# Optimization experiments

Hardware: AMD Instinct MI355X
Metric: run time of the kernel (lower is better)

Reference implementation:

```python
import jax, jax.numpy as jnp
import numpy as np

N_EMBD = 1024
N_HEAD = 16
HEAD_DIM = N_EMBD // N_HEAD


def setup_inputs() -> dict:
    key = jax.random.key(0)
    ks = jax.random.split(key, 9)
    B, T, C = 2, 2048, N_EMBD
    s = 1.0 / np.sqrt(C)
    inp = {
        "x": jax.random.normal(ks[0], (B, T, C), dtype=jnp.float32),
        "Wq": jax.random.normal(ks[1], (C, C), dtype=jnp.float32) * s,
        "bq": jnp.zeros((C,), dtype=jnp.float32),
        "Wk": jax.random.normal(ks[2], (C, C), dtype=jnp.float32) * s,
        "bk": jnp.zeros((C,), dtype=jnp.float32),
        "Wv": jax.random.normal(ks[3], (C, C), dtype=jnp.float32) * s,
        "bv": jnp.zeros((C,), dtype=jnp.float32),
        "Wo": jax.random.normal(ks[4], (C, C), dtype=jnp.float32) * s,
        "bo": jnp.zeros((C,), dtype=jnp.float32),
    }
    return inp


def reference(x, Wq, bq, Wk, bk, Wv, bv, Wo, bo):
    B, T, C = x.shape
    H, D = N_HEAD, HEAD_DIM
    # projections (torch Linear: x @ W^T + b)
    q = (x @ Wq.T + bq).reshape(B, T, H, D).transpose(0, 2, 1, 3)  # [B,H,T,D]
    k = (x @ Wk.T + bk).reshape(B, T, H, D).transpose(0, 2, 1, 3)
    v = (x @ Wv.T + bv).reshape(B, T, H, D).transpose(0, 2, 1, 3)
    scores = jnp.einsum("bhqd,bhkd->bhqk", q, k) / jnp.sqrt(jnp.asarray(D, x.dtype))
    causal = jnp.tril(jnp.ones((T, T), dtype=bool))
    scores = jnp.where(causal[None, None], scores, jnp.asarray(-jnp.inf, x.dtype))
    weights = jax.nn.softmax(scores, axis=-1)  # [B,H,T,T]
    attended = jnp.einsum("bhqk,bhkd->bhqd", weights, v)
    attended = attended.transpose(0, 2, 1, 3).reshape(B, T, C)
    return attended @ Wo.T + bo
```

## Files before the change

kernel.cpp:

```cpp
#include <hip/hip_runtime.h>

typedef unsigned short u16;
typedef __attribute__((ext_vector_type(8))) __bf16 bf16x8;
typedef __attribute__((ext_vector_type(4))) float f32x4;
typedef __attribute__((ext_vector_type(4))) unsigned int u32x4;

#define MFMA16(a, b, c) __builtin_amdgcn_mfma_f32_16x16x32_bf16(a, b, c, 0, 0, 0)

__device__ __forceinline__ u16 f2bf(float f) {
    unsigned u = __float_as_uint(f);
    u = (u + 0x7FFFu + ((u >> 16) & 1u)) >> 16;
    return (u16)u;
}

__device__ __forceinline__ void gl_lds16(const u16* g, u16* l) {
    __builtin_amdgcn_global_load_lds(
        (const __attribute__((address_space(1))) unsigned int*)g,
        (__attribute__((address_space(3))) unsigned int*)l, 16, 0, 0);
}

static constexpr int Bv = 2, Tv = 2048, Cv = 1024, Hv = 16, Dv = 64;
static constexpr int Mv = Bv * Tv;

static constexpr size_t OFF_XB = 0;
static constexpr size_t OFF_WQ = 4194304;
static constexpr size_t OFF_WK = OFF_WQ + 1048576;
static constexpr size_t OFF_WV = OFF_WK + 1048576;
static constexpr size_t OFF_WO = OFF_WV + 1048576;
static constexpr size_t OFF_Q  = OFF_WO + 1048576;
static constexpr size_t OFF_K  = OFF_Q + 4194304;
static constexpr size_t OFF_VT = OFF_K + 4194304;
static constexpr size_t OFF_A  = OFF_VT + 4194304;

__global__ __launch_bounds__(256) void convert_all(
    const float* __restrict__ x,
    const float* __restrict__ wq, const float* __restrict__ wk,
    const float* __restrict__ wv, const float* __restrict__ wo,
    u16* __restrict__ dst)
{
    int i4 = blockIdx.x * blockDim.x + threadIdx.x;
    if (i4 >= 2097152) return;
    int idx = i4 * 4;
    const float* src; int off;
    if (idx < 4194304) { src = x; off = idx; }
    else {
        int rel = idx - 4194304;
        int j = rel >> 20;
        off = rel & 1048575;
        src = (j == 0) ? wq : (j == 1) ? wk : (j == 2) ? wv : wo;
    }
    float4 v = *(const float4*)(src + off);
    ushort4 o;
    o.x = f2bf(v.x); o.y = f2bf(v.y); o.z = f2bf(v.z); o.w = f2bf(v.w);
    *(ushort4*)(dst + idx) = o;
}

template <bool OUT_BF16, bool ROWBIAS>
__device__ __forceinline__ void gemm128_b64(
    u16* __restrict__ lA0, u16* __restrict__ lB0,
    u16* __restrict__ lA1, u16* __restrict__ lB1,
    const u16* __restrict__ A, const u16* __restrict__ Wt,
    const float* __restrict__ bias, void* __restrict__ outp,
    int m0, int n0, int N, int K)
{
    const int tid  = threadIdx.x;
    const int lane = tid & 63, w = tid >> 6;
    const int quad = lane >> 4, lm = lane & 15;
    const int wm = (w & 1) * 64, wn = (w >> 1) * 32;
    const int rowi = lane >> 3, seg = lane & 7;

    f32x4 zero = {0.f, 0.f, 0.f, 0.f};
    f32x4 acc[4][2];
    #pragma unroll
    for (int mt = 0; mt < 4; mt++)
        #pragma unroll
        for (int nt = 0; nt < 2; nt++) acc[mt][nt] = zero;

    auto stage = [&](u16* dA, u16* dB, int k0) __attribute__((always_inline)) {
        #pragma unroll
        for (int i = 0; i < 2; i++) {
            int rbase = w * 16 + i * 8;
            int row = rbase + rowi;
            int gseg = seg ^ (row & 7);
            gl_lds16(A  + (size_t)(m0 + row) * K + k0 + gseg * 8, &dA[rbase * 64]);
            gl_lds16(Wt + (size_t)(n0 + row) * K + k0 + gseg * 8, &dB[rbase * 64]);
        }
    };
    auto compute = [&](const u16* sA, const u16* sB) __attribute__((always_inline)) {
        #pragma unroll
        for (int ks = 0; ks < 2; ks++) {
            const int swz = ((ks * 4 + quad) ^ (lm & 7)) * 8;
            bf16x8 af[4], bf[2];
            #pragma unroll
            for (int mt = 0; mt < 4; mt++)
                af[mt] = *(const bf16x8*)&sA[(wm + mt * 16 + lm) * 64 + swz];
            #pragma unroll
            for (int nt = 0; nt < 2; nt++)
                bf[nt] = *(const bf16x8*)&sB[(wn + nt * 16 + lm) * 64 + swz];
            #pragma unroll
            for (int mt = 0; mt < 4; mt++)
                #pragma unroll
                for (int nt = 0; nt < 2; nt++)
                    acc[mt][nt] = MFMA16(af[mt], bf[nt], acc[mt][nt]);
        }
    };

    const int NT = K >> 6;
    stage(lA0, lB0, 0);
    stage(lA1, lB1, 64);
    for (int t = 0; t < NT; ++t) {
        if (t + 1 < NT) asm volatile("s_waitcnt vmcnt(4)" ::: "memory");
        else            asm volatile("s_waitcnt vmcnt(0)" ::: "memory");
        __builtin_amdgcn_s_barrier();
        u16* sA = (t & 1) ? lA1 : lA0;
        u16* sB = (t & 1) ? lB1 : lB0;
        compute(sA, sB);
        asm volatile("s_waitcnt lgkmcnt(0)" ::: "memory");
        __builtin_amdgcn_s_barrier();
        if (t + 2 < NT) stage(sA, sB, (t + 2) << 6);
    }

    #pragma unroll
    for (int nt = 0; nt < 2; nt++) {
        int col = n0 + wn + nt * 16 + lm;
        float cb = ROWBIAS ? 0.f : bias[col];
        #pragma unroll
        for (int mt = 0; mt < 4; mt++) {
            #pragma unroll
            for (int r = 0; r < 4; r++) {
                int row = m0 + wm + mt * 16 + quad * 4 + r;
                float v = acc[mt][nt][r] + (ROWBIAS ? bias[row] : cb);
                if (OUT_BF16) ((u16*)outp)[(size_t)row * N + col] = f2bf(v);
                else          ((float*)outp)[(size_t)row * N + col] = v;
            }
        }
    }
}

__global__ __launch_bounds__(512) void gemm_qkv(
    const u16* __restrict__ A,
    const u16* __restrict__ Wq, const u16* __restrict__ Wk, const u16* __restrict__ Wv,
    const float* __restrict__ bq, const float* __restrict__ bk, const float* __restrict__ bv,
    u16* __restrict__ Q, u16* __restrict__ K, u16* __restrict__ VT)
{
    __shared__ u16 lA0[128 * 64];
    __shared__ u16 lB0[128 * 64];
    __shared__ u16 lA1[128 * 64];
    __shared__ u16 lB1[128 * 64];

    int bid = blockIdx.x;
    int sw  = (bid & 7) * 96 + (bid >> 3);
    int g2  = sw >> 5;
    int row = sw & 31;
    int which = g2 >> 3, col = g2 & 7;

    if (which == 0) {
        gemm128_b64<true, false>(lA0, lB0, lA1, lB1, A, Wq, bq, Q, row * 128, col * 128, Cv, Cv);
    } else if (which == 1) {
        gemm128_b64<true, false>(lA0, lB0, lA1, lB1, A, Wk, bk, K, row * 128, col * 128, Cv, Cv);
    } else {
        gemm128_b64<true, true>(lA0, lB0, lA1, lB1, Wv, A, bv, VT, col * 128, row * 128, Mv, Cv);
    }
}

__global__ __launch_bounds__(512) void gemm_o64(
    const u16* __restrict__ A, const u16* __restrict__ Wt,
    const float* __restrict__ bias, float* __restrict__ outp)
{
    __shared__ u16 lA0[128 * 64];
    __shared__ u16 lA1[128 * 64];
    __shared__ u16 lB0[64 * 64];
    __shared__ u16 lB1[64 * 64];

    const int tid  = threadIdx.x;
    const int lane = tid & 63, w = tid >> 6;
    const int quad = lane >> 4, lm = lane & 15;
    const int wm = (w & 3) * 32, wn = (w >> 2) * 32;

    int bid = blockIdx.x;
    int sw  = (bid & 7) * 64 + (bid >> 3);
    const int n0 = (sw >> 5) * 64;
    const int m0 = (sw & 31) * 128;
    const int K = Cv;
    const int rowi = lane >> 3, seg = lane & 7;

    f32x4 zero = {0.f, 0.f, 0.f, 0.f};
    f32x4 acc[2][2];
    #pragma unroll
    for (int mt = 0; mt < 2; mt++)
        #pragma unroll
        for (int nt = 0; nt < 2; nt++) acc[mt][nt] = zero;

    auto stage = [&](u16* dA, u16* dB, int k0) __attribute__((always_inline)) {
        #pragma unroll
        for (int i = 0; i < 2; i++) {
            int rbase = w * 16 + i * 8;
            int row = rbase + rowi;
            int gseg = seg ^ (row & 7);
            gl_lds16(A + (size_t)(m0 + row) * K + k0 + gseg * 8, &dA[rbase * 64]);
        }
        {
            int rbase = w * 8, row = rbase + rowi;
            gl_lds16(Wt + (size_t)(n0 + row) * K + k0 + ((seg ^ (row & 7))) * 8, &dB[rbase * 64]);
        }
    };
    auto compute = [&](const u16* sA, const u16* sB) __attribute__((always_inline)) {
        #pragma unroll
        for (int ks = 0; ks < 2; ks++) {
            const int swz = ((ks * 4 + quad) ^ (lm & 7)) * 8;
            bf16x8 af[2], bf[2];
            #pragma unroll
            for (int mt = 0; mt < 2; mt++)
                af[mt] = *(const bf16x8*)&sA[(wm + mt * 16 + lm) * 64 + swz];
            #pragma unroll
            for (int nt = 0; nt < 2; nt++)
                bf[nt] = *(const bf16x8*)&sB[(wn + nt * 16 + lm) * 64 + swz];
            #pragma unroll
            for (int mt = 0; mt < 2; mt++)
                #pragma unroll
                for (int nt = 0; nt < 2; nt++)
                    acc[mt][nt] = MFMA16(af[mt], bf[nt], acc[mt][nt]);
        }
    };

    const int NT = K >> 6;
    stage(lA0, lB0, 0);
    stage(lA1, lB1, 64);
    for (int t = 0; t < NT; ++t) {
        if (t + 1 < NT) asm volatile("s_waitcnt vmcnt(3)" ::: "memory");
        else            asm volatile("s_waitcnt vmcnt(0)" ::: "memory");
        __builtin_amdgcn_s_barrier();
        u16* sA = (t & 1) ? lA1 : lA0;
        u16* sB = (t & 1) ? lB1 : lB0;
        compute(sA, sB);
        asm volatile("s_waitcnt lgkmcnt(0)" ::: "memory");
        __builtin_amdgcn_s_barrier();
        if (t + 2 < NT) stage(sA, sB, (t + 2) << 6);
    }

    #pragma unroll
    for (int nt = 0; nt < 2; nt++) {
        int col = n0 + wn + nt * 16 + lm;
        float bvv = bias[col];
        #pragma unroll
        for (int mt = 0; mt < 2; mt++) {
            #pragma unroll
            for (int r = 0; r < 4; r++) {
                int row = m0 + wm + mt * 16 + quad * 4 + r;
                outp[(size_t)row * Cv + col] = acc[mt][nt][r] + bvv;
            }
        }
    }
}

__global__ __launch_bounds__(512) void attn(
    const u16* __restrict__ Qp, const u16* __restrict__ Kp,
    const u16* __restrict__ VTg, u16* __restrict__ Op)
{
    __shared__ u16 lK[2][64 * 64];
    __shared__ u16 lVT[2][64 * 64];
    __shared__ u16 lP[8][32][72];

    const int tid  = threadIdx.x;
    const int lane = tid & 63, w = tid >> 6;
    const int g = w >> 2, wl = w & 3;
    const int quad = lane >> 4, lm = lane & 15;

    const int idx  = blockIdx.x;
    const int half = idx >> 8;
    const int grp  = idx & 255;
    const int bh   = (half << 4) | (grp >> 4);
    const int j    = grp & 15;
    const int qt   = half ? j : 15 - j;
    const int h = bh & 15, b = bh >> 4;

    const int qb = qt * 128;
    const size_t headoff = (size_t)b * Tv * Cv + (size_t)h * Dv;
    const size_t vthead  = (size_t)h * 64 * Mv + (size_t)b * Tv;

    bf16x8 qf[2][2];
    #pragma unroll
    for (int nt = 0; nt < 2; nt++) {
        const u16* qptr = Qp + headoff + (size_t)(qb + wl * 32 + nt * 16 + lm) * Cv + quad * 8;
        qf[0][nt] = *(const bf16x8*)(qptr);
        qf[1][nt] = *(const bf16x8*)(qptr + 32);
    }

    f32x4 zero = {0.f, 0.f, 0.f, 0.f};
    f32x4 oacc[2][4];
    #pragma unroll
    for (int mt = 0; mt < 2; mt++)
        #pragma unroll
        for (int nt = 0; nt < 4; nt++) oacc[mt][nt] = zero;
    float Lp[2] = {0.f, 0.f};

    const float SC = 0.18033688011112042f;
    const int rowi = lane >> 3, seg = lane & 7;

    auto stage = [&](int kt) {
        const int k0 = kt * 64;
        #pragma unroll
        for (int hf = 0; hf < 2; hf++) {
            int rbase = wl * 16 + hf * 8;
            int row = rbase + rowi;
            int gseg = seg ^ (row & 7);
            gl_lds16(Kp + headoff + (size_t)(k0 + row) * Cv + gseg * 8, &lK[g][rbase * 64]);
            gl_lds16(VTg + vthead + (size_t)row * Mv + k0 + gseg * 8, &lVT[g][rbase * 64]);
        }
    };

    auto body = [&](int kt, bool domask) __attribute__((always_inline)) {
        const int k0 = kt * 64;
        f32x4 stt[4][2];
        #pragma unroll
        for (int mt = 0; mt < 4; mt++)
            #pragma unroll
            for (int nt = 0; nt < 2; nt++) stt[mt][nt] = zero;
        #pragma unroll
        for (int ks = 0; ks < 2; ks++) {
            #pragma unroll
            for (int mt = 0; mt < 4; mt++) {
                bf16x8 kf = *(const bf16x8*)
                    &lK[g][(mt * 16 + lm) * 64 + (((ks * 4 + quad) ^ (lm & 7)) * 8)];
                #pragma unroll
                for (int nt = 0; nt < 2; nt++)
                    stt[mt][nt] = MFMA16(kf, qf[ks][nt], stt[mt][nt]);
            }
        }
        #pragma unroll
        for (int mt = 0; mt < 4; mt++) {
            #pragma unroll
            for (int nt = 0; nt < 2; nt++) {
                const int keyb = k0 + mt * 16 + quad * 4;
                const int qrow = qb + wl * 32 + nt * 16 + lm;
                float e0 = __builtin_amdgcn_exp2f(fmaf(stt[mt][nt][0], SC, -16.f));
                float e1 = __builtin_amdgcn_exp2f(fmaf(stt[mt][nt][1], SC, -16.f));
                float e2 = __builtin_amdgcn_exp2f(fmaf(stt[mt][nt][2], SC, -16.f));
                float e3 = __builtin_amdgcn_exp2f(fmaf(stt[mt][nt][3], SC, -16.f));
                if (domask) {
                    if (keyb + 0 > qrow) e0 = 0.f;
                    if (keyb + 1 > qrow) e1 = 0.f;
                    if (keyb + 2 > qrow) e2 = 0.f;
                    if (keyb + 3 > qrow) e3 = 0.f;
                }
                Lp[nt] += e0 + e1 + e2 + e3;
                ushort4 pk;
                pk.x = (u16)(__float_as_uint(e0) >> 16);
                pk.y = (u16)(__float_as_uint(e1) >> 16);
                pk.z = (u16)(__float_as_uint(e2) >> 16);
                pk.w = (u16)(__float_as_uint(e3) >> 16);
                *(ushort4*)&lP[w][nt * 16 + lm][mt * 16 + quad * 4] = pk;
            }
        }
        #pragma unroll
        for (int ks = 0; ks < 2; ks++) {
            bf16x8 pf[2];
            #pragma unroll
            for (int mt = 0; mt < 2; mt++)
                pf[mt] = *(const bf16x8*)&lP[w][mt * 16 + lm][ks * 32 + quad * 8];
            #pragma unroll
            for (int nt = 0; nt < 4; nt++) {
                bf16x8 vf = *(const bf16x8*)
                    &lVT[g][(nt * 16 + lm) * 64 + (((ks * 4 + quad) ^ (lm & 7)) * 8)];
                #pragma unroll
                for (int mt = 0; mt < 2; mt++)
                    oacc[mt][nt] = MFMA16(pf[mt], vf, oacc[mt][nt]);
            }
        }
    };

    for (int i = 0; i < qt; i++) {
        if (i) __syncthreads();
        stage(2 * i + g);
        __syncthreads();
        body(2 * i + g, false);
    }
    if (qt) __syncthreads();
    stage(2 * qt + g);
    __syncthreads();
    body(2 * qt + g, true);
    __syncthreads();

    float* lO = (float*)&lP[0][0][0];
    float* lL = lO + 32 * 256;
    const int t = tid & 255;
    if (g == 1) {
        #pragma unroll
        for (int mt = 0; mt < 2; mt++)
            #pragma unroll
            for (int nt = 0; nt < 4; nt++)
                #pragma unroll
                for (int r = 0; r < 4; r++)
                    lO[(mt * 16 + nt * 4 + r) * 256 + t] = oacc[mt][nt][r];
        lL[t] = Lp[0];
        lL[256 + t] = Lp[1];
    }
    __syncthreads();
    if (g == 0) {
        #pragma unroll
        for (int mt = 0; mt < 2; mt++)
            #pragma unroll
            for (int nt = 0; nt < 4; nt++)
                #pragma unroll
                for (int r = 0; r < 4; r++)
                    oacc[mt][nt][r] += lO[(mt * 16 + nt * 4 + r) * 256 + t];
        Lp[0] += lL[t];
        Lp[1] += lL[256 + t];

        float Lred[2];
        #pragma unroll
        for (int nt = 0; nt < 2; nt++) {
            float L = Lp[nt];
            L += __shfl_xor(L, 16, 64);
            L += __shfl_xor(L, 32, 64);
            Lred[nt] = 1.0f / L;
        }
        #pragma unroll
        for (int mt = 0; mt < 2; mt++) {
            float inv[4];
            #pragma unroll
            for (int r = 0; r < 4; r++)
                inv[r] = __shfl(Lred[mt], (lane & 48) | (quad * 4 + r), 64);
            #pragma unroll
            for (int nt = 0; nt < 4; nt++) {
                #pragma unroll
                for (int r = 0; r < 4; r++) {
                    int row = qb + wl * 32 + mt * 16 + quad * 4 + r;
                    Op[headoff + (size_t)row * Cv + nt * 16 + lm] = f2bf(oacc[mt][nt][r] * inv[r]);
                }
            }
        }
    }
}

extern "C" void kernel_launch(void* const* d_in, const int* in_sizes, int n_in,
                              void* d_out, int out_size, void* d_ws, size_t ws_size,
                              hipStream_t stream) {
    const float* x  = (const float*)d_in[0];
    const float* Wq = (const float*)d_in[1];
    const float* bq = (const float*)d_in[2];
    const float* Wk = (const float*)d_in[3];
    const float* bk = (const float*)d_in[4];
    const float* Wv = (const float*)d_in[5];
    const float* bv = (const float*)d_in[6];
    const float* Wo = (const float*)d_in[7];
    const float* bo = (const float*)d_in[8];
    u16* ws = (u16*)d_ws;

    convert_all<<<8192, 256, 0, stream>>>(x, Wq, Wk, Wv, Wo, ws);

    gemm_qkv<<<768, 512, 0, stream>>>(
        ws + OFF_XB, ws + OFF_WQ, ws + OFF_WK, ws + OFF_WV,
        bq, bk, bv, ws + OFF_Q, ws + OFF_K, ws + OFF_VT);

    attn<<<512, 512, 0, stream>>>(ws + OFF_Q, ws + OFF_K, ws + OFF_VT, ws + OFF_A);

    gemm_o64<<<512, 512, 0, stream>>>(ws + OFF_A, ws + OFF_WO, bo, (float*)d_out);
}
```

Before: 173.3 us.

## Restructure QKV GEMM to 256-thread blocks with K=32 steps and packed LDS

```diff
diff --git a/kernel.cpp b/kernel.cpp
--- a/kernel.cpp
+++ b/kernel.cpp
@@ -56,7 +56,7 @@
 }
 
 template <bool OUT_BF16, bool ROWBIAS>
-__device__ __forceinline__ void gemm128_b64(
+__device__ __forceinline__ void gemm128_b32(
     u16* __restrict__ lA0, u16* __restrict__ lB0,
     u16* __restrict__ lA1, u16* __restrict__ lB1,
     const u16* __restrict__ A, const u16* __restrict__ Wt,
@@ -66,62 +66,60 @@
     const int tid  = threadIdx.x;
     const int lane = tid & 63, w = tid >> 6;
     const int quad = lane >> 4, lm = lane & 15;
-    const int wm = (w & 1) * 64, wn = (w >> 1) * 32;
+    const int wm = (w & 1) * 64, wn = (w >> 1) * 64;
+    const int h4A = (w & 1) * 4, h4B = ((w >> 1) & 1) * 4;
     const int rowi = lane >> 3, seg = lane & 7;
+    const int raw = seg ^ rowi;
+    const int hh  = raw >> 2, qq = raw & 3;
 
     f32x4 zero = {0.f, 0.f, 0.f, 0.f};
-    f32x4 acc[4][2];
+    f32x4 acc[4][4];
     #pragma unroll
     for (int mt = 0; mt < 4; mt++)
         #pragma unroll
-        for (int nt = 0; nt < 2; nt++) acc[mt][nt] = zero;
+        for (int nt = 0; nt < 4; nt++) acc[mt][nt] = zero;
 
     auto stage = [&](u16* dA, u16* dB, int k0) __attribute__((always_inline)) {
         #pragma unroll
-        for (int i = 0; i < 2; i++) {
-            int rbase = w * 16 + i * 8;
-            int row = rbase + rowi;
-            int gseg = seg ^ (row & 7);
-            gl_lds16(A  + (size_t)(m0 + row) * K + k0 + gseg * 8, &dA[rbase * 64]);
-            gl_lds16(Wt + (size_t)(n0 + row) * K + k0 + gseg * 8, &dB[rbase * 64]);
+        for (int j = 0; j < 2; j++) {
+            int pr0 = w * 16 + j * 8;
+            int gr  = pr0 + rowi + (hh << 6);
+            gl_lds16(A  + (size_t)(m0 + gr) * K + k0 + qq * 8, &dA[pr0 * 64]);
+            gl_lds16(Wt + (size_t)(n0 + gr) * K + k0 + qq * 8, &dB[pr0 * 64]);
         }
     };
     auto compute = [&](const u16* sA, const u16* sB) __attribute__((always_inline)) {
-        #pragma unroll
-        for (int ks = 0; ks < 2; ks++) {
-            const int swz = ((ks * 4 + quad) ^ (lm & 7)) * 8;
-            bf16x8 af[4], bf[2];
-            #pragma unroll
-            for (int mt = 0; mt < 4; mt++)
-                af[mt] = *(const bf16x8*)&sA[(wm + mt * 16 + lm) * 64 + swz];
-            #pragma unroll
-            for (int nt = 0; nt < 2; nt++)
-                bf[nt] = *(const bf16x8*)&sB[(wn + nt * 16 + lm) * 64 + swz];
-            #pragma unroll
-            for (int mt = 0; mt < 4; mt++)
-                #pragma unroll
-                for (int nt = 0; nt < 2; nt++)
-                    acc[mt][nt] = MFMA16(af[mt], bf[nt], acc[mt][nt]);
-        }
-    };
-
-    const int NT = K >> 6;
+        bf16x8 af[4], bf[4];
+        #pragma unroll
+        for (int mt = 0; mt < 4; mt++)
+            af[mt] = *(const bf16x8*)&sA[(mt * 16 + lm) * 64 + (((h4A + quad) ^ (lm & 7)) * 8)];
+        #pragma unroll
+        for (int nt = 0; nt < 4; nt++)
+            bf[nt] = *(const bf16x8*)&sB[(nt * 16 + lm) * 64 + (((h4B + quad) ^ (lm & 7)) * 8)];
+        #pragma unroll
+        for (int mt = 0; mt < 4; mt++)
+            #pragma unroll
+            for (int nt = 0; nt < 4; nt++)
+                acc[mt][nt] = MFMA16(af[mt], bf[nt], acc[mt][nt]);
+    };
+
+    const int NT = K >> 5;
     stage(lA0, lB0, 0);
-    stage(lA1, lB1, 64);
+    stage(lA1, lB1, 32);
     for (int t = 0; t < NT; ++t) {
         if (t + 1 < NT) asm volatile("s_waitcnt vmcnt(4)" ::: "memory");
         else            asm volatile("s_waitcnt vmcnt(0)" ::: "memory");
         __builtin_amdgcn_s_barrier();
-        u16* sA = (t & 1) ? lA1 : lA0;
-        u16* sB = (t & 1) ? lB1 : lB0;
+        const u16* sA = (t & 1) ? lA1 : lA0;
+        const u16* sB = (t & 1) ? lB1 : lB0;
         compute(sA, sB);
         asm volatile("s_waitcnt lgkmcnt(0)" ::: "memory");
         __builtin_amdgcn_s_barrier();
-        if (t + 2 < NT) stage(sA, sB, (t + 2) << 6);
-    }
-
-    #pragma unroll
-    for (int nt = 0; nt < 2; nt++) {
+        if (t + 2 < NT) stage((t & 1) ? lA1 : lA0, (t & 1) ? lB1 : lB0, (t + 2) << 5);
+    }
+
+    #pragma unroll
+    for (int nt = 0; nt < 4; nt++) {
         int col = n0 + wn + nt * 16 + lm;
         float cb = ROWBIAS ? 0.f : bias[col];
         #pragma unroll
@@ -137,16 +135,16 @@
     }
 }
 
-__global__ __launch_bounds__(512) void gemm_qkv(
+__global__ __launch_bounds__(256, 3) void gemm_qkv(
     const u16* __restrict__ A,
     const u16* __restrict__ Wq, const u16* __restrict__ Wk, const u16* __restrict__ Wv,
     const float* __restrict__ bq, const float* __restrict__ bk, const float* __restrict__ bv,
     u16* __restrict__ Q, u16* __restrict__ K, u16* __restrict__ VT)
 {
-    __shared__ u16 lA0[128 * 64];
-    __shared__ u16 lB0[128 * 64];
-    __shared__ u16 lA1[128 * 64];
-    __shared__ u16 lB1[128 * 64];
+    __shared__ u16 lA0[64 * 64];
+    __shared__ u16 lB0[64 * 64];
+    __shared__ u16 lA1[64 * 64];
+    __shared__ u16 lB1[64 * 64];
 
     int bid = blockIdx.x;
     int sw  = (bid & 7) * 96 + (bid >> 3);
@@ -155,11 +153,11 @@
     int which = g2 >> 3, col = g2 & 7;
 
     if (which == 0) {
-        gemm128_b64<true, false>(lA0, lB0, lA1, lB1, A, Wq, bq, Q, row * 128, col * 128, Cv, Cv);
+        gemm128_b32<true, false>(lA0, lB0, lA1, lB1, A, Wq, bq, Q, row * 128, col * 128, Cv, Cv);
     } else if (which == 1) {
-        gemm128_b64<true, false>(lA0, lB0, lA1, lB1, A, Wk, bk, K, row * 128, col * 128, Cv, Cv);
+        gemm128_b32<true, false>(lA0, lB0, lA1, lB1, A, Wk, bk, K, row * 128, col * 128, Cv, Cv);
     } else {
-        gemm128_b64<true, true>(lA0, lB0, lA1, lB1, Wv, A, bv, VT, col * 128, row * 128, Mv, Cv);
+        gemm128_b32<true, true>(lA0, lB0, lA1, lB1, Wv, A, bv, VT, col * 128, row * 128, Mv, Cv);
     }
 }
 
@@ -449,7 +447,7 @@
 
     convert_all<<<8192, 256, 0, stream>>>(x, Wq, Wk, Wv, Wo, ws);
 
-    gemm_qkv<<<768, 512, 0, stream>>>(
+    gemm_qkv<<<768, 256, 0, stream>>>(
         ws + OFF_XB, ws + OFF_WQ, ws + OFF_WK, ws + OFF_WV,
         bq, bk, bv, ws + OFF_Q, ws + OFF_K, ws + OFF_VT);
 
```

Result: slower. 177.1 us (+2.2%).
